# Kernel optimization log

Hardware: AMD Instinct MI355X
Metric: run time of the kernel (lower is better)

The kernel has to match this reference:

```python
import jax, jax.numpy as jnp
import numpy as np

DIM = 512
HEADS = 8
DIM_HEAD = 64
HIDDEN = HEADS * DIM_HEAD  # 512
SCALE = DIM_HEAD ** -0.5
EPS = 1e-5


def setup_inputs() -> dict:
    key = jax.random.key(0)
    ks = jax.random.split(key, 6)
    B, N = 4, 8192
    x = jax.random.normal(ks[0], (B, DIM, N), dtype=jnp.float32)
    ln_w = jnp.ones((DIM,), dtype=jnp.float32)
    ln_b = jnp.zeros((DIM,), dtype=jnp.float32)
    # stored as (in, out) so y = x @ W
    w_qkv = jax.random.normal(ks[1], (DIM, 3 * HIDDEN), dtype=jnp.float32) * (DIM ** -0.5)
    w_out = jax.random.normal(ks[2], (HIDDEN, DIM), dtype=jnp.float32) * (HIDDEN ** -0.5)
    b_out = jnp.zeros((DIM,), dtype=jnp.float32)
    return {"x": x, "ln_w": ln_w, "ln_b": ln_b, "w_qkv": w_qkv, "w_out": w_out, "b_out": b_out}


def _forward(x, ln_w, ln_b, w_qkv, w_out, b_out):
    B, D, N = x.shape
    h = jnp.swapaxes(x, 1, 2)  # b n d
    # LayerNorm over last dim
    mu = jnp.mean(h, axis=-1, keepdims=True)
    var = jnp.var(h, axis=-1, keepdims=True)
    h = (h - mu) * jax.lax.rsqrt(var + EPS) * ln_w + ln_b
    qkv = h @ w_qkv  # b n 3*hidden
    q, k, v = jnp.split(qkv, 3, axis=-1)
    # b n (h d) -> b h n d
    reshape = lambda t: jnp.swapaxes(t.reshape(B, N, HEADS, DIM_HEAD), 1, 2)
    q, k, v = reshape(q), reshape(k), reshape(v)
    q = jax.nn.softmax(q * SCALE, axis=-2)  # softmax over tokens n
    k = jax.nn.softmax(k, axis=-1)          # softmax over features d
    context = jnp.einsum('bhnd,bhne->bhde', k, v)  # small d x e per head
    out = jnp.einsum('bhde,bhnd->bhen', context, q)
    # b h e n -> b n (h e)
    out = jnp.swapaxes(out, 1, 3).reshape(B, N, HIDDEN)  # bhen -> bneh? careful: need (h e)
    # redo correctly: bhen -> b n h e -> b n (h e)
    # (the line above gives b n e h; compute properly instead)
    return out


def reference(x, ln_w, ln_b, w_qkv, w_out, b_out):
    B, D, N = x.shape
    h = jnp.swapaxes(x, 1, 2)  # b n d
    mu = jnp.mean(h, axis=-1, keepdims=True)
    var = jnp.var(h, axis=-1, keepdims=True)
    h = (h - mu) * jax.lax.rsqrt(var + EPS) * ln_w + ln_b
    qkv = h @ w_qkv  # b n 3*hidden
    q, k, v = jnp.split(qkv, 3, axis=-1)
    reshape = lambda t: jnp.swapaxes(t.reshape(B, N, HEADS, DIM_HEAD), 1, 2)  # b h n d
    q, k, v = reshape(q), reshape(k), reshape(v)
    q = jax.nn.softmax(q * SCALE, axis=-2)  # over tokens
    k = jax.nn.softmax(k, axis=-1)          # over head-dim
    context = jnp.einsum('bhnd,bhne->bhde', k, v)
    out = jnp.einsum('bhde,bhnd->bnhe', context, q)  # b n h e
    out = out.reshape(B, N, HIDDEN)  # (h e) concatenated per head
    out = out @ w_out + b_out  # b n dim
    return jnp.swapaxes(out, 1, 2)  # b dim n
```

## Files before the change

### kernel.cpp

```cpp
#include <hip/hip_runtime.h>

#define B_   4
#define N_   8192
#define D_   512
#define NH   8
#define DH   64
#define HID  512

typedef unsigned short u16;
typedef __attribute__((ext_vector_type(8))) short  bf16x8;
typedef __attribute__((ext_vector_type(8))) unsigned short u16x8;
typedef __attribute__((ext_vector_type(4))) float  f32x4;

__device__ __forceinline__ float bf2f(u16 u) {
  unsigned int i = ((unsigned int)u) << 16;
  return __builtin_bit_cast(float, i);
}
__device__ __forceinline__ u16 f2bf(float f) {
  unsigned int i = __builtin_bit_cast(unsigned int, f);
  i += 0x7fff + ((i >> 16) & 1);
  return (u16)(i >> 16);
}

#define GLOAD16(g, l) \
  __builtin_amdgcn_global_load_lds((const __attribute__((address_space(1))) void*)(g), \
                                   (__attribute__((address_space(3))) void*)(l), 16, 0, 0)

__global__ __launch_bounds__(256) void transpose_f2b(const float* __restrict__ in,
                                                     u16* __restrict__ out,
                                                     int rows, int cols) {
  __shared__ u16 tile[64][65];
  int c0 = blockIdx.x * 64, r0 = blockIdx.y * 64;
  int t = threadIdx.x;
  int rl = t >> 6, cl = t & 63;
#pragma unroll
  for (int i = 0; i < 16; i++) {
    int r = i * 4 + rl;
    tile[r][cl] = f2bf(in[(long)(r0 + r) * cols + c0 + cl]);
  }
  __syncthreads();
  int c4 = t >> 6, rr = t & 63;
#pragma unroll
  for (int i = 0; i < 16; i++) {
    int c = i * 4 + c4;
    out[(long)(c0 + c) * rows + r0 + rr] = tile[rr][c];
  }
}

__global__ __launch_bounds__(256) void ln_kernel(const float* __restrict__ x,
                                                 const float* __restrict__ lw,
                                                 const float* __restrict__ lb,
                                                 u16* __restrict__ h) {
  __shared__ u16 xs[32 * 520];
  __shared__ float red[2][8][32];
  __shared__ float murs[2][32];
  __shared__ float lws[512], lbs[512];
  int b = blockIdx.y, n0 = blockIdx.x * 32;
  int t = threadIdx.x;
  lws[t] = lw[t]; lws[t + 256] = lw[t + 256];
  lbs[t] = lb[t]; lbs[t + 256] = lb[t + 256];
  int tok = t & 31, dp = t >> 5;
  const float* xp = x + (long)b * D_ * N_ + n0 + tok;
  float s = 0.f, s2 = 0.f;
#pragma unroll 8
  for (int i = 0; i < 64; i++) {
    int d = dp * 64 + i;
    float v = xp[(long)d * N_];
    s += v; s2 += v * v;
    xs[tok * 520 + d] = f2bf(v);
  }
  red[0][dp][tok] = s; red[1][dp][tok] = s2;
  __syncthreads();
  if (t < 32) {
    float S1 = 0.f, S2 = 0.f;
#pragma unroll
    for (int i = 0; i < 8; i++) { S1 += red[0][i][t]; S2 += red[1][i][t]; }
    float mu = S1 * (1.0f / 512.0f);
    float var = S2 * (1.0f / 512.0f) - mu * mu;
    murs[0][t] = mu; murs[1][t] = rsqrtf(var + 1e-5f);
  }
  __syncthreads();
  int row = t >> 3, seg = t & 7;
  float mu = murs[0][row], rs = murs[1][row];
  u16* hp = h + ((long)b * N_ + n0 + row) * D_;
  const u16* xr = xs + row * 520;
#pragma unroll
  for (int c = 0; c < 8; c++) {
    int d0 = c * 64 + seg * 8;
    u16x8 in8 = *(const u16x8*)(xr + d0);
    u16x8 o;
#pragma unroll
    for (int i = 0; i < 8; i++) {
      int d = d0 + i;
      o[i] = f2bf((bf2f(in8[i]) - mu) * rs * lws[d] + lbs[d]);
    }
    *(u16x8*)(hp + d0) = o;
  }
}

__global__ __launch_bounds__(256) void gemm1(const u16* __restrict__ A,
                                             const u16* __restrict__ B,
                                             u16* __restrict__ qexp,
                                             u16* __restrict__ expkT,
                                             u16* __restrict__ vT,
                                             float* __restrict__ S,
                                             float* __restrict__ Z) {
  const int K = 512;
  __shared__ u16 As[128 * 32];
  __shared__ u16 Bs[128 * 32];
  __shared__ u16 Cs[128 * 136];
  int m0 = blockIdx.y * 128, n0 = blockIdx.x * 128;
  int tid = threadIdx.x, wave = tid >> 6, lane = tid & 63;
  int l15 = lane & 15, qd = lane >> 4;

  int ra0 = tid >> 2,          qa0 = (tid & 3) ^ ((ra0 >> 1) & 3);
  int ra1 = (tid + 256) >> 2,  qa1 = (tid & 3) ^ ((ra1 >> 1) & 3);
  const u16* gA0 = A + (long)(m0 + ra0) * K + qa0 * 8;
  const u16* gA1 = A + (long)(m0 + ra1) * K + qa1 * 8;
  const u16* gB0 = B + (long)(n0 + ra0) * K + qa0 * 8;
  const u16* gB1 = B + (long)(n0 + ra1) * K + qa1 * 8;
  u16* lA0 = As + wave * 512;
  u16* lA1 = As + 2048 + wave * 512;
  u16* lB0 = Bs + wave * 512;
  u16* lB1 = Bs + 2048 + wave * 512;

  int wm = wave & 1, wn = wave >> 1;
  int aoff[4], boff[4];
#pragma unroll
  for (int i = 0; i < 4; i++) {
    int r = wm * 64 + i * 16 + l15;
    aoff[i] = r * 32 + ((qd ^ ((r >> 1) & 3)) * 8);
    int rb = wn * 64 + i * 16 + l15;
    boff[i] = rb * 32 + ((qd ^ ((rb >> 1) & 3)) * 8);
  }

  f32x4 zero = {0.f, 0.f, 0.f, 0.f};
  f32x4 acc[4][4];
#pragma unroll
  for (int i = 0; i < 4; i++)
#pragma unroll
    for (int j = 0; j < 4; j++) acc[i][j] = zero;

  for (int k0 = 0; k0 < K; k0 += 32) {
    __syncthreads();
    GLOAD16(gA0 + k0, lA0);
    GLOAD16(gA1 + k0, lA1);
    GLOAD16(gB0 + k0, lB0);
    GLOAD16(gB1 + k0, lB1);
    __syncthreads();
    bf16x8 af[4], bf[4];
#pragma unroll
    for (int i = 0; i < 4; i++) {
      af[i] = *(const bf16x8*)(As + aoff[i]);
      bf[i] = *(const bf16x8*)(Bs + boff[i]);
    }
#pragma unroll
    for (int i = 0; i < 4; i++)
#pragma unroll
      for (int j = 0; j < 4; j++)
        acc[i][j] = __builtin_amdgcn_mfma_f32_16x16x32_bf16(af[i], bf[j], acc[i][j], 0, 0, 0);
  }

  int third = n0 >> 9;
  int n0t = n0 & 511;
  int b = m0 >> 13;
  int tloc = m0 & 8191;

  if (third == 0) {
#pragma unroll
    for (int i = 0; i < 4; i++)
#pragma unroll
      for (int j = 0; j < 4; j++)
#pragma unroll
        for (int r = 0; r < 4; r++) acc[i][j][r] = __expf(acc[i][j][r] * 0.125f);
#pragma unroll
    for (int j = 0; j < 4; j++) {
      float ps = 0.f;
#pragma unroll
      for (int i = 0; i < 4; i++)
#pragma unroll
        for (int r = 0; r < 4; r++) ps += acc[i][j][r];
      ps += __shfl_xor(ps, 16);
      ps += __shfl_xor(ps, 32);
      if (qd == 0) atomicAdd(S + b * 512 + n0t + wn * 64 + j * 16 + l15, ps);
    }
  } else if (third == 1) {
#pragma unroll
    for (int i = 0; i < 4; i++)
#pragma unroll
      for (int j = 0; j < 4; j++)
#pragma unroll
        for (int r = 0; r < 4; r++) acc[i][j][r] = __expf(acc[i][j][r]);
    int head = (n0t >> 6) + wn;
#pragma unroll
    for (int i = 0; i < 4; i++)
#pragma unroll
      for (int r = 0; r < 4; r++) {
        float rs = acc[i][0][r] + acc[i][1][r] + acc[i][2][r] + acc[i][3][r];
        rs += __shfl_xor(rs, 1);
        rs += __shfl_xor(rs, 2);
        rs += __shfl_xor(rs, 4);
        rs += __shfl_xor(rs, 8);
        if (l15 == 0)
          atomicAdd(Z + ((long)b * NH + head) * 8192 + tloc + wm * 64 + i * 16 + qd * 4 + r, rs);
      }
  }

  if (third == 0) {
#pragma unroll
    for (int i = 0; i < 4; i++)
#pragma unroll
      for (int r = 0; r < 4; r++)
#pragma unroll
        for (int j = 0; j < 4; j++)
          Cs[(wm * 64 + i * 16 + qd * 4 + r) * 136 + wn * 64 + j * 16 + l15] =
              f2bf(acc[i][j][r]);
  } else {
#pragma unroll
    for (int i = 0; i < 4; i++)
#pragma unroll
      for (int r = 0; r < 4; r++)
#pragma unroll
        for (int j = 0; j < 4; j++)
          Cs[(wn * 64 + j * 16 + l15) * 136 + wm * 64 + i * 16 + qd * 4 + r] =
              f2bf(acc[i][j][r]);
  }
  __syncthreads();

  u16* dst; long ldg;
  if (third == 0)      { dst = qexp  + ((long)b * N_ + tloc) * 512 + n0t;  ldg = 512; }
  else if (third == 1) { dst = expkT + ((long)b * 512 + n0t) * 8192 + tloc; ldg = 8192; }
  else                 { dst = vT    + ((long)b * 512 + n0t) * 8192 + tloc; ldg = 8192; }

  int seg = lane & 7;
#pragma unroll
  for (int outer = 0; outer < 2; outer++)
#pragma unroll
    for (int rr = 0; rr < 2; rr++) {
      int row = outer * 64 + wave * 16 + rr * 8 + (lane >> 3);
      const u16* src = Cs + row * 136;
      u16* dp = dst + (long)row * ldg;
#pragma unroll
      for (int p = 0; p < 2; p++)
        *(uint4*)(dp + p * 64 + seg * 8) = *(const uint4*)(src + p * 64 + seg * 8);
    }
}

__global__ __launch_bounds__(256) void zrecip(float* __restrict__ Z) {
  int i = blockIdx.x * 256 + threadIdx.x;
  Z[i] = 1.0f / Z[i];
}

__global__ __launch_bounds__(256) void ctx_kernel(const u16* __restrict__ expkT,
                                                  const u16* __restrict__ vT,
                                                  const float* __restrict__ Zr,
                                                  float* __restrict__ ctx) {
  __shared__ u16 As[64 * 128];
  __shared__ u16 Bs[64 * 128];
  int kc = blockIdx.x, hh = blockIdx.y, b = blockIdx.z;
  int t = threadIdx.x, w = t >> 6, l = t & 63, l15 = l & 15, qd = l >> 4;
  long nbase = (long)kc * 512;
  const u16* Abase = expkT + ((long)b * 512 + hh * 64) * 8192 + nbase;
  const u16* Bbase = vT   + ((long)b * 512 + hh * 64) * 8192 + nbase;
  const float* Zb = Zr + ((long)b * NH + hh) * 8192 + nbase;

  f32x4 zero = {0.f, 0.f, 0.f, 0.f};
  f32x4 acc[4] = {zero, zero, zero, zero};

  int brow = t >> 2;
  for (int s = 0; s < 4; s++) {
    long ko = (long)s * 128;
    __syncthreads();
#pragma unroll
    for (int si = 0; si < 4; si++) {
      int qq = si * 4 + w;
      int row = qq * 4 + (l >> 4);
      int gs = (l & 15) ^ (row & 15);
      GLOAD16(Abase + (long)row * 8192 + ko + gs * 8, As + qq * 512);
    }
    {
      const u16* src = Bbase + (long)brow * 8192 + ko;
#pragma unroll
      for (int cc = 0; cc < 4; cc++) {
        int c = (t & 3) * 4 + cc;
        u16x8 v8 = *(const u16x8*)(src + c * 8);
        float4 z0 = *(const float4*)(Zb + ko + c * 8);
        float4 z1 = *(const float4*)(Zb + ko + c * 8 + 4);
        u16x8 o;
        o[0] = f2bf(bf2f(v8[0]) * z0.x); o[1] = f2bf(bf2f(v8[1]) * z0.y);
        o[2] = f2bf(bf2f(v8[2]) * z0.z); o[3] = f2bf(bf2f(v8[3]) * z0.w);
        o[4] = f2bf(bf2f(v8[4]) * z1.x); o[5] = f2bf(bf2f(v8[5]) * z1.y);
        o[6] = f2bf(bf2f(v8[6]) * z1.z); o[7] = f2bf(bf2f(v8[7]) * z1.w);
        *(u16x8*)(Bs + brow * 128 + ((c ^ (brow & 15)) * 8)) = o;
      }
    }
    __syncthreads();
#pragma unroll
    for (int kk = 0; kk < 4; kk++) {
      int ar = w * 16 + l15;
      bf16x8 af = *(const bf16x8*)(As + ar * 128 + (((kk * 4 + qd) ^ (ar & 15)) * 8));
#pragma unroll
      for (int j = 0; j < 4; j++) {
        int br = j * 16 + l15;
        bf16x8 bf8 = *(const bf16x8*)(Bs + br * 128 + (((kk * 4 + qd) ^ (br & 15)) * 8));
        acc[j] = __builtin_amdgcn_mfma_f32_16x16x32_bf16(af, bf8, acc[j], 0, 0, 0);
      }
    }
  }
  float* cp = ctx + ((long)(b * NH + hh)) * DH * DH;
#pragma unroll
  for (int j = 0; j < 4; j++)
#pragma unroll
    for (int r = 0; r < 4; r++)
      atomicAdd(cp + (w * 16 + qd * 4 + r) * 64 + j * 16 + l15, acc[j][r]);
}

__global__ __launch_bounds__(256) void mprime(const float* __restrict__ ctx,
                                              const float* __restrict__ wout,
                                              const float* __restrict__ S,
                                              u16* __restrict__ Mt) {
  __shared__ float ws[64 * 65];
  __shared__ float cs[64 * 65];
  int dt = blockIdx.x, hh = blockIdx.y, b = blockIdx.z;
  int t = threadIdx.x;
  {
    int e = t >> 2;
#pragma unroll
    for (int ii = 0; ii < 4; ii++) {
      int col = (t & 3) * 16 + ii * 4;
      float4 v = *(const float4*)(wout + (long)(hh * 64 + e) * 512 + dt * 64 + col);
      ws[e * 65 + col] = v.x; ws[e * 65 + col + 1] = v.y;
      ws[e * 65 + col + 2] = v.z; ws[e * 65 + col + 3] = v.w;
      float4 c = *(const float4*)(ctx + ((long)(b * NH + hh)) * 4096 + (long)e * 64 + col);
      cs[e * 65 + col] = c.x; cs[e * 65 + col + 1] = c.y;
      cs[e * 65 + col + 2] = c.z; cs[e * 65 + col + 3] = c.w;
    }
  }
  __syncthreads();
  int dol = t & 63, dg = t >> 6;
#pragma unroll
  for (int dd = 0; dd < 16; dd++) {
    int d = dg * 16 + dd;
    float v = 0.f;
#pragma unroll 8
    for (int e = 0; e < 64; e++) v += cs[d * 65 + e] * ws[e * 65 + dol];
    float sv = S[b * 512 + hh * 64 + d];
    Mt[(long)b * 262144 + (long)(dt * 64 + dol) * 512 + hh * 64 + d] = f2bf(v / sv);
  }
}

__global__ __launch_bounds__(256) void gemm_tn_f(const u16* __restrict__ A,
                                                 const u16* __restrict__ B,
                                                 float* __restrict__ C,
                                                 const float* __restrict__ bias,
                                                 int K, int ldc,
                                                 long sA, long sB, long sC) {
  __shared__ u16 As[128 * 32];
  __shared__ u16 Bs[128 * 32];
  __shared__ float Cf[64 * 133];
  long bz = blockIdx.z;
  A += bz * sA; B += bz * sB; C += bz * sC;
  int m0 = blockIdx.x * 128, n0 = blockIdx.y * 128;
  int tid = threadIdx.x, wave = tid >> 6, lane = tid & 63;
  int l15 = lane & 15, qd = lane >> 4;

  int ra0 = tid >> 2,          qa0 = (tid & 3) ^ ((ra0 >> 1) & 3);
  int ra1 = (tid + 256) >> 2,  qa1 = (tid & 3) ^ ((ra1 >> 1) & 3);
  const u16* gA0 = A + (long)(m0 + ra0) * K + qa0 * 8;
  const u16* gA1 = A + (long)(m0 + ra1) * K + qa1 * 8;
  const u16* gB0 = B + (long)(n0 + ra0) * K + qa0 * 8;
  const u16* gB1 = B + (long)(n0 + ra1) * K + qa1 * 8;
  u16* lA0 = As + wave * 512;
  u16* lA1 = As + 2048 + wave * 512;
  u16* lB0 = Bs + wave * 512;
  u16* lB1 = Bs + 2048 + wave * 512;

  int wm = wave & 1, wn = wave >> 1;
  int aoff[4], boff[4];
#pragma unroll
  for (int i = 0; i < 4; i++) {
    int r = wm * 64 + i * 16 + l15;
    aoff[i] = r * 32 + ((qd ^ ((r >> 1) & 3)) * 8);
    int rb = wn * 64 + i * 16 + l15;
    boff[i] = rb * 32 + ((qd ^ ((rb >> 1) & 3)) * 8);
  }

  f32x4 zero = {0.f, 0.f, 0.f, 0.f};
  f32x4 acc[4][4];
#pragma unroll
  for (int i = 0; i < 4; i++)
#pragma unroll
    for (int j = 0; j < 4; j++) acc[i][j] = zero;

  for (int k0 = 0; k0 < K; k0 += 32) {
    __syncthreads();
    GLOAD16(gA0 + k0, lA0);
    GLOAD16(gA1 + k0, lA1);
    GLOAD16(gB0 + k0, lB0);
    GLOAD16(gB1 + k0, lB1);
    __syncthreads();
    bf16x8 af[4], bf[4];
#pragma unroll
    for (int i = 0; i < 4; i++) {
      af[i] = *(const bf16x8*)(As + aoff[i]);
      bf[i] = *(const bf16x8*)(Bs + boff[i]);
    }
#pragma unroll
    for (int i = 0; i < 4; i++)
#pragma unroll
      for (int j = 0; j < 4; j++)
        acc[i][j] = __builtin_amdgcn_mfma_f32_16x16x32_bf16(af[i], bf[j], acc[i][j], 0, 0, 0);
  }

#pragma unroll
  for (int half = 0; half < 2; half++) {
    __syncthreads();
    if (wm == half) {
#pragma unroll
      for (int i = 0; i < 4; i++)
#pragma unroll
        for (int r = 0; r < 4; r++) {
          int rl = i * 16 + qd * 4 + r;
          float bv = bias[m0 + half * 64 + rl];
#pragma unroll
          for (int j = 0; j < 4; j++)
            Cf[rl * 133 + wn * 64 + j * 16 + l15] = acc[i][j][r] + bv;
        }
    }
    __syncthreads();
#pragma unroll
    for (int z = 0; z < 2; z++) {
      int rl = z * 32 + (tid >> 3);
      int seg = tid & 7;
      float* dp = C + (long)(m0 + half * 64 + rl) * ldc + n0;
      const float* src = Cf + rl * 133;
#pragma unroll
      for (int p = 0; p < 4; p++)
        *(float4*)(dp + p * 32 + seg * 4) = *(const float4*)(src + p * 32 + seg * 4);
    }
  }
}

extern "C" void kernel_launch(void* const* d_in, const int* in_sizes, int n_in,
                              void* d_out, int out_size, void* d_ws, size_t ws_size,
                              hipStream_t stream) {
  const float* x    = (const float*)d_in[0];
  const float* lnw  = (const float*)d_in[1];
  const float* lnb  = (const float*)d_in[2];
  const float* wqkv = (const float*)d_in[3];
  const float* wout = (const float*)d_in[4];
  const float* bout = (const float*)d_in[5];
  float* out = (float*)d_out;
  char* ws = (char*)d_ws;

  u16*  h     = (u16*)(ws + 0L);
  u16*  qexp  = (u16*)(ws + 33554432L);
  u16*  expkT = (u16*)(ws + 67108864L);
  u16*  vT    = (u16*)(ws + 100663296L);
  u16*  wqkvT = (u16*)(ws + 134217728L);
  u16*  Mt    = (u16*)(ws + 134217728L);
  float* S    = (float*)(ws + 136314880L);
  float* ctx  = (float*)(ws + 0L);
  float* Z    = (float*)d_out;

  hipMemsetAsync(S, 0, 4 * 512 * 4, stream);
  hipMemsetAsync(Z, 0, (long)B_ * NH * 8192 * 4, stream);

  transpose_f2b<<<dim3(24, 8), 256, 0, stream>>>(wqkv, wqkvT, 512, 1536);

  ln_kernel<<<dim3(256, 4), 256, 0, stream>>>(x, lnw, lnb, h);

  gemm1<<<dim3(12, 256), 256, 0, stream>>>(h, wqkvT, qexp, expkT, vT, S, Z);

  zrecip<<<dim3(1024), 256, 0, stream>>>(Z);

  hipMemsetAsync(ctx, 0, 4 * 8 * 64 * 64 * 4, stream);

  ctx_kernel<<<dim3(16, 8, 4), 256, 0, stream>>>(expkT, vT, Z, ctx);

  mprime<<<dim3(8, 8, 4), 256, 0, stream>>>(ctx, wout, S, Mt);

  gemm_tn_f<<<dim3(4, 64, 4), 256, 0, stream>>>(Mt, qexp, out, bout, 512, 8192,
                                                262144L, (long)8192 * 512, (long)512 * 8192);
}
```

Before: 312.4 us.

## Double-buffer LDS k-loop and remap block ids for XCD locality in GEMMs

Both GEMM kernels now prefetch the next K tile into a second LDS buffer while the current tile runs through MFMA, with one barrier per iteration instead of two. Shared memory is unioned into one buffer that is reused for the epilogue staging. Block indices are remapped so consecutive blocks that share A/B tiles land on the same XCD (bid&7 grouping), aiming at better L2 reuse. This relies on hardcoded grid sizes (12x384, 4x64xB) and manual waitcnt sequencing, and the union must fit the epilogue tile.

```diff
diff --git a/kernel.cpp b/kernel.cpp
--- a/kernel.cpp
+++ b/kernel.cpp
@@ -106,10 +106,13 @@
                                              float* __restrict__ S,
                                              float* __restrict__ Z) {
   const int K = 512;
-  __shared__ u16 As[128 * 32];
-  __shared__ u16 Bs[128 * 32];
-  __shared__ u16 Cs[128 * 136];
-  int m0 = blockIdx.y * 128, n0 = blockIdx.x * 128;
+  __shared__ alignas(16) u16 smem[17408];
+
+  int bid = blockIdx.y * 12 + blockIdx.x;
+  int wid = (bid & 7) * 384 + (bid >> 3);
+  int bx = wid % 12, by = wid / 12;
+  int m0 = by * 128, n0 = bx * 128;
+
   int tid = threadIdx.x, wave = tid >> 6, lane = tid & 63;
   int l15 = lane & 15, qd = lane >> 4;
 
@@ -119,10 +122,6 @@
   const u16* gA1 = A + (long)(m0 + ra1) * K + qa1 * 8;
   const u16* gB0 = B + (long)(n0 + ra0) * K + qa0 * 8;
   const u16* gB1 = B + (long)(n0 + ra1) * K + qa1 * 8;
-  u16* lA0 = As + wave * 512;
-  u16* lA1 = As + 2048 + wave * 512;
-  u16* lB0 = Bs + wave * 512;
-  u16* lB1 = Bs + 2048 + wave * 512;
 
   int wm = wave & 1, wn = wave >> 1;
   int aoff[4], boff[4];
@@ -141,25 +140,56 @@
 #pragma unroll
     for (int j = 0; j < 4; j++) acc[i][j] = zero;
 
-  for (int k0 = 0; k0 < K; k0 += 32) {
-    __syncthreads();
-    GLOAD16(gA0 + k0, lA0);
-    GLOAD16(gA1 + k0, lA1);
-    GLOAD16(gB0 + k0, lB0);
-    GLOAD16(gB1 + k0, lB1);
-    __syncthreads();
+#define STAGE1(buf, kk) { \
+    u16* dA = smem + (buf) * 8192 + wave * 512; \
+    u16* dB = smem + (buf) * 8192 + 4096 + wave * 512; \
+    GLOAD16(gA0 + (kk), dA); GLOAD16(gA1 + (kk), dA + 2048); \
+    GLOAD16(gB0 + (kk), dB); GLOAD16(gB1 + (kk), dB + 2048); }
+
+  STAGE1(0, 0);
+  asm volatile("s_waitcnt vmcnt(0)" ::: "memory");
+  __builtin_amdgcn_s_barrier();
+
+#pragma unroll
+  for (int it = 0; it < 15; it++) {
+    const int cur = it & 1, nxt = cur ^ 1;
+    STAGE1(nxt, (it + 1) * 32);
+    const u16* Ac = smem + cur * 8192;
+    const u16* Bc = smem + cur * 8192 + 4096;
     bf16x8 af[4], bf[4];
 #pragma unroll
-    for (int i = 0; i < 4; i++) {
-      af[i] = *(const bf16x8*)(As + aoff[i]);
-      bf[i] = *(const bf16x8*)(Bs + boff[i]);
+    for (int q = 0; q < 4; q++) {
+      af[q] = *(const bf16x8*)(Ac + aoff[q]);
+      bf[q] = *(const bf16x8*)(Bc + boff[q]);
     }
 #pragma unroll
     for (int i = 0; i < 4; i++)
 #pragma unroll
       for (int j = 0; j < 4; j++)
         acc[i][j] = __builtin_amdgcn_mfma_f32_16x16x32_bf16(af[i], bf[j], acc[i][j], 0, 0, 0);
-  }
+    asm volatile("s_waitcnt vmcnt(0) lgkmcnt(0)" ::: "memory");
+    __builtin_amdgcn_s_barrier();
+  }
+  {
+    const u16* Ac = smem + 8192;
+    const u16* Bc = smem + 8192 + 4096;
+    bf16x8 af[4], bf[4];
+#pragma unroll
+    for (int q = 0; q < 4; q++) {
+      af[q] = *(const bf16x8*)(Ac + aoff[q]);
+      bf[q] = *(const bf16x8*)(Bc + boff[q]);
+    }
+#pragma unroll
+    for (int i = 0; i < 4; i++)
+#pragma unroll
+      for (int j = 0; j < 4; j++)
+        acc[i][j] = __builtin_amdgcn_mfma_f32_16x16x32_bf16(af[i], bf[j], acc[i][j], 0, 0, 0);
+  }
+  asm volatile("s_waitcnt lgkmcnt(0)" ::: "memory");
+  __builtin_amdgcn_s_barrier();
+#undef STAGE1
+
+  u16* Cs = smem;
 
   int third = n0 >> 9;
   int n0t = n0 & 511;
@@ -355,12 +385,17 @@
                                                  const float* __restrict__ bias,
                                                  int K, int ldc,
                                                  long sA, long sB, long sC) {
-  __shared__ u16 As[128 * 32];
-  __shared__ u16 Bs[128 * 32];
-  __shared__ float Cf[64 * 133];
-  long bz = blockIdx.z;
+  __shared__ alignas(16) u16 smem[17408];
+  float* Cf = (float*)smem;
+
+  int bid = (blockIdx.z * gridDim.y + blockIdx.y) * gridDim.x + blockIdx.x;
+  int wid = (bid & 7) * 128 + (bid >> 3);
+  int mx = wid & 3;
+  int ny = (wid >> 2) & 63;
+  long bz = wid >> 8;
   A += bz * sA; B += bz * sB; C += bz * sC;
-  int m0 = blockIdx.x * 128, n0 = blockIdx.y * 128;
+  int m0 = mx * 128, n0 = ny * 128;
+
   int tid = threadIdx.x, wave = tid >> 6, lane = tid & 63;
   int l15 = lane & 15, qd = lane >> 4;
 
@@ -370,10 +405,6 @@
   const u16* gA1 = A + (long)(m0 + ra1) * K + qa1 * 8;
   const u16* gB0 = B + (long)(n0 + ra0) * K + qa0 * 8;
   const u16* gB1 = B + (long)(n0 + ra1) * K + qa1 * 8;
-  u16* lA0 = As + wave * 512;
-  u16* lA1 = As + 2048 + wave * 512;
-  u16* lB0 = Bs + wave * 512;
-  u16* lB1 = Bs + 2048 + wave * 512;
 
   int wm = wave & 1, wn = wave >> 1;
   int aoff[4], boff[4];
@@ -392,25 +423,54 @@
 #pragma unroll
     for (int j = 0; j < 4; j++) acc[i][j] = zero;
 
-  for (int k0 = 0; k0 < K; k0 += 32) {
-    __syncthreads();
-    GLOAD16(gA0 + k0, lA0);
-    GLOAD16(gA1 + k0, lA1);
-    GLOAD16(gB0 + k0, lB0);
-    GLOAD16(gB1 + k0, lB1);
-    __syncthreads();
+#define STAGE2(buf, kk) { \
+    u16* dA = smem + (buf) * 8192 + wave * 512; \
+    u16* dB = smem + (buf) * 8192 + 4096 + wave * 512; \
+    GLOAD16(gA0 + (kk), dA); GLOAD16(gA1 + (kk), dA + 2048); \
+    GLOAD16(gB0 + (kk), dB); GLOAD16(gB1 + (kk), dB + 2048); }
+
+  STAGE2(0, 0);
+  asm volatile("s_waitcnt vmcnt(0)" ::: "memory");
+  __builtin_amdgcn_s_barrier();
+
+#pragma unroll
+  for (int it = 0; it < 15; it++) {
+    const int cur = it & 1, nxt = cur ^ 1;
+    STAGE2(nxt, (it + 1) * 32);
+    const u16* Ac = smem + cur * 8192;
+    const u16* Bc = smem + cur * 8192 + 4096;
     bf16x8 af[4], bf[4];
 #pragma unroll
-    for (int i = 0; i < 4; i++) {
-      af[i] = *(const bf16x8*)(As + aoff[i]);
-      bf[i] = *(const bf16x8*)(Bs + boff[i]);
+    for (int q = 0; q < 4; q++) {
+      af[q] = *(const bf16x8*)(Ac + aoff[q]);
+      bf[q] = *(const bf16x8*)(Bc + boff[q]);
     }
 #pragma unroll
     for (int i = 0; i < 4; i++)
 #pragma unroll
       for (int j = 0; j < 4; j++)
         acc[i][j] = __builtin_amdgcn_mfma_f32_16x16x32_bf16(af[i], bf[j], acc[i][j], 0, 0, 0);
-  }
+    asm volatile("s_waitcnt vmcnt(0) lgkmcnt(0)" ::: "memory");
+    __builtin_amdgcn_s_barrier();
+  }
+  {
+    const u16* Ac = smem + 8192;
+    const u16* Bc = smem + 8192 + 4096;
+    bf16x8 af[4], bf[4];
+#pragma unroll
+    for (int q = 0; q < 4; q++) {
+      af[q] = *(const bf16x8*)(Ac + aoff[q]);
+      bf[q] = *(const bf16x8*)(Bc + boff[q]);
+    }
+#pragma unroll
+    for (int i = 0; i < 4; i++)
+#pragma unroll
+      for (int j = 0; j < 4; j++)
+        acc[i][j] = __builtin_amdgcn_mfma_f32_16x16x32_bf16(af[i], bf[j], acc[i][j], 0, 0, 0);
+  }
+  asm volatile("s_waitcnt lgkmcnt(0)" ::: "memory");
+  __builtin_amdgcn_s_barrier();
+#undef STAGE2
 
 #pragma unroll
   for (int half = 0; half < 2; half++) {
```

Measured after the change: 286.8 us. 1.09x faster.
